# Optimization experiments

Hardware: AMD Instinct MI355X
Metric: run time of the kernel (lower is better)

## Reference

```python
import jax, jax.numpy as jnp
import numpy as np

B, L, D = 4, 2048, 1024
H, KD, VD = 16, 64, 64
EPS = 1e-5


def setup_inputs() -> dict:
    key = jax.random.key(0)
    ks = jax.random.split(key, 12)
    s_in = 1.0 / np.sqrt(D)
    s_out = 1.0 / np.sqrt(H * VD)
    return {
        "queries": jax.random.normal(ks[0], (B, L, D), dtype=jnp.float32),
        "Wq": jax.random.uniform(ks[1], (D, H * KD), jnp.float32, -s_in, s_in),
        "bq": jax.random.uniform(ks[2], (H * KD,), jnp.float32, -s_in, s_in),
        "Wk": jax.random.uniform(ks[3], (D, H * KD), jnp.float32, -s_in, s_in),
        "bk": jax.random.uniform(ks[4], (H * KD,), jnp.float32, -s_in, s_in),
        "Wv": jax.random.uniform(ks[5], (D, H * VD), jnp.float32, -s_in, s_in),
        "bv": jax.random.uniform(ks[6], (H * VD,), jnp.float32, -s_in, s_in),
        "Wo": jax.random.uniform(ks[7], (H * VD, D), jnp.float32, -s_out, s_out),
        "bo": jax.random.uniform(ks[8], (D,), jnp.float32, -s_out, s_out),
        "gamma": jnp.ones((D,), jnp.float32),
        "beta": jnp.zeros((D,), jnp.float32),
    }


def reference(queries, Wq, bq, Wk, bk, Wv, bv, Wo, bo, gamma, beta):
    # QKV projections -> [B, L, H, head_dim]
    q = (queries @ Wq + bq).reshape(B, L, H, KD)
    k = (queries @ Wk + bk).reshape(B, L, H, KD)
    v = (queries @ Wv + bv).reshape(B, L, H, VD)
    # scaled dot-product attention per head: scores [B, H, Lq, Lk]
    scores = jnp.einsum("bqhd,bkhd->bhqk", q, k) / np.sqrt(KD).astype(np.float32)
    attn = jax.nn.softmax(scores, axis=-1)
    out = jnp.einsum("bhqk,bkhd->bqhd", attn, v).reshape(B, L, H * VD)
    # out projection (dropout is identity in eval), residual + LayerNorm
    res = out @ Wo + bo + queries
    mu = jnp.mean(res, axis=-1, keepdims=True)
    var = jnp.var(res, axis=-1, keepdims=True)
    return (res - mu) / jnp.sqrt(var + EPS) * gamma + beta
```

## Files before the change

### kernel.cpp

```cpp
#include <hip/hip_runtime.h>
#include <hip/hip_bf16.h>

#define BATCH 4
#define SEQ   2048
#define DIM   1024
#define NHEAD 16
#define HDIM  64
#define EPS_LN 1e-5f
#define QSCALE 0.18033688011112042f

typedef __attribute__((ext_vector_type(8))) short short8;
typedef __attribute__((ext_vector_type(4))) float f32x4;

__device__ __forceinline__ unsigned short f2bf(float x) {
    __hip_bfloat16 h = __float2bfloat16(x);
    return *reinterpret_cast<unsigned short*>(&h);
}
__device__ __forceinline__ unsigned int pack2bf(float a, float b) {
    __hip_bfloat162 h = __float22bfloat162_rn(float2{a, b});
    return *reinterpret_cast<unsigned int*>(&h);
}

__device__ __forceinline__ void gl_lds16(const void* g, void* l) {
    __builtin_amdgcn_global_load_lds(
        (const __attribute__((address_space(1))) unsigned int*)g,
        (__attribute__((address_space(3))) unsigned int*)l,
        16, 0, 0);
}

__global__ __launch_bounds__(256) void convert_bf16(const float* __restrict__ in,
                                                    unsigned short* __restrict__ out)
{
    const int i = blockIdx.x * 256 + threadIdx.x;
    float4 v = ((const float4*)in)[i];
    ushort4 u;
    u.x = f2bf(v.x); u.y = f2bf(v.y); u.z = f2bf(v.z); u.w = f2bf(v.w);
    ((ushort4*)out)[i] = u;
}

__global__ __launch_bounds__(256) void transpose_convert4(const float* __restrict__ W0,
                                                          const float* __restrict__ W1,
                                                          const float* __restrict__ W2,
                                                          const float* __restrict__ W3,
                                                          unsigned short* __restrict__ Wqkvt,
                                                          unsigned short* __restrict__ Wot)
{
    __shared__ float Ts[64][65];
    const int z = blockIdx.z;
    const float* W = (z == 0) ? W0 : (z == 1) ? W1 : (z == 2) ? W2 : W3;
    unsigned short* Wt = (z == 3) ? Wot : (Wqkvt + (size_t)z * DIM * DIM);

    const int k0 = blockIdx.y * 64, n0 = blockIdx.x * 64;
    const int t = threadIdx.x;
    const int lr = t >> 2, lq = t & 3;

#pragma unroll
    for (int i = 0; i < 4; i++) {
        float4 v = *(const float4*)(W + (size_t)(k0 + lr) * DIM + n0 + (lq * 4 + i) * 4);
        Ts[lr][(lq * 4 + i) * 4 + 0] = v.x;
        Ts[lr][(lq * 4 + i) * 4 + 1] = v.y;
        Ts[lr][(lq * 4 + i) * 4 + 2] = v.z;
        Ts[lr][(lq * 4 + i) * 4 + 3] = v.w;
    }
    __syncthreads();
#pragma unroll
    for (int i = 0; i < 4; i++) {
        const int c = lq * 16 + i * 4;
        ushort4 u;
        u.x = f2bf(Ts[c + 0][lr]);
        u.y = f2bf(Ts[c + 1][lr]);
        u.z = f2bf(Ts[c + 2][lr]);
        u.w = f2bf(Ts[c + 3][lr]);
        *(ushort4*)(Wt + (size_t)(n0 + lr) * DIM + k0 + c) = u;
    }
}

__global__ __launch_bounds__(256) void gemm_qkv(const unsigned short* __restrict__ A,
                                                const unsigned short* __restrict__ Bt,
                                                const float* __restrict__ bq,
                                                const float* __restrict__ bk,
                                                const float* __restrict__ bv,
                                                unsigned short* __restrict__ Qbf,
                                                unsigned short* __restrict__ Kbf,
                                                unsigned short* __restrict__ Vtb)
{
    __shared__ __attribute__((aligned(16))) unsigned short As[128 * 32];
    __shared__ __attribute__((aligned(16))) unsigned short Bs[128 * 32];

    const int tid = threadIdx.x;
    const int w = tid >> 6, lane = tid & 63;
    const int col = lane & 15, quad = lane >> 4;
    const int wm = (w >> 1) * 64, wn = (w & 1) * 64;
    const int m0 = blockIdx.y * 128, n0 = blockIdx.x * 128;

    f32x4 acc[4][4] = {};
    const int srow = tid >> 2, sc4 = tid & 3;

    for (int k0 = 0; k0 < DIM; k0 += 32) {
        __syncthreads();
#pragma unroll
        for (int it = 0; it < 2; it++) {
            gl_lds16(A  + (size_t)(m0 + srow + it * 64) * DIM + k0 + sc4 * 8,
                     (char*)As + w * 1024 + it * 4096);
            gl_lds16(Bt + (size_t)(n0 + srow + it * 64) * DIM + k0 + sc4 * 8,
                     (char*)Bs + w * 1024 + it * 4096);
        }
        __syncthreads();

        short8 af[4], bf[4];
#pragma unroll
        for (int mt = 0; mt < 4; mt++) af[mt] = *(short8*)&As[(wm + mt * 16 + col) * 32 + quad * 8];
#pragma unroll
        for (int nt = 0; nt < 4; nt++) bf[nt] = *(short8*)&Bs[(wn + nt * 16 + col) * 32 + quad * 8];

#pragma unroll
        for (int mt = 0; mt < 4; mt++)
#pragma unroll
            for (int nt = 0; nt < 4; nt++)
                acc[mt][nt] = __builtin_amdgcn_mfma_f32_16x16x32_bf16(af[mt], bf[nt], acc[mt][nt], 0, 0, 0);
    }

    const int sector = n0 >> 10;
    const float* bias = (sector == 0) ? bq : (sector == 1) ? bk : bv;

#pragma unroll
    for (int nt = 0; nt < 4; nt++) {
        const int n = n0 + wn + nt * 16 + col;
        const int nloc = n - (sector << 10);
        const float bvv = bias[nloc];
#pragma unroll
        for (int mt = 0; mt < 4; mt++) {
            const int mbase = m0 + wm + mt * 16 + quad * 4;
            if (sector == 0) {
#pragma unroll
                for (int r = 0; r < 4; r++)
                    Qbf[(size_t)(mbase + r) * DIM + nloc] = f2bf((acc[mt][nt][r] + bvv) * QSCALE);
            } else if (sector == 1) {
#pragma unroll
                for (int r = 0; r < 4; r++)
                    Kbf[(size_t)(mbase + r) * DIM + nloc] = f2bf(acc[mt][nt][r] + bvv);
            } else {
                const int h = nloc >> 6, d = nloc & 63;
                const int b = mbase >> 11, l = mbase & 2047;
                ushort4 u;
                u.x = f2bf(acc[mt][nt][0] + bvv);
                u.y = f2bf(acc[mt][nt][1] + bvv);
                u.z = f2bf(acc[mt][nt][2] + bvv);
                u.w = f2bf(acc[mt][nt][3] + bvv);
                *(ushort4*)(Vtb + ((size_t)((b * NHEAD + h) * HDIM + d)) * SEQ + l) = u;
            }
        }
    }
}

__global__ __launch_bounds__(256) void gemm_out(const unsigned short* __restrict__ A,
                                                const unsigned short* __restrict__ Bt,
                                                const float* __restrict__ bias,
                                                const float* __restrict__ resid,
                                                float* __restrict__ Cout)
{
    __shared__ __attribute__((aligned(16))) unsigned short As[128 * 32];
    __shared__ __attribute__((aligned(16))) unsigned short Bs[128 * 32];

    const int tid = threadIdx.x;
    const int w = tid >> 6, lane = tid & 63;
    const int col = lane & 15, quad = lane >> 4;
    const int wm = (w >> 1) * 64, wn = (w & 1) * 64;
    const int m0 = blockIdx.y * 128, n0 = blockIdx.x * 128;

    f32x4 acc[4][4] = {};
    const int srow = tid >> 2, sc4 = tid & 3;

    for (int k0 = 0; k0 < DIM; k0 += 32) {
        __syncthreads();
#pragma unroll
        for (int it = 0; it < 2; it++) {
            gl_lds16(A  + (size_t)(m0 + srow + it * 64) * DIM + k0 + sc4 * 8,
                     (char*)As + w * 1024 + it * 4096);
            gl_lds16(Bt + (size_t)(n0 + srow + it * 64) * DIM + k0 + sc4 * 8,
                     (char*)Bs + w * 1024 + it * 4096);
        }
        __syncthreads();

        short8 af[4], bf[4];
#pragma unroll
        for (int mt = 0; mt < 4; mt++) af[mt] = *(short8*)&As[(wm + mt * 16 + col) * 32 + quad * 8];
#pragma unroll
        for (int nt = 0; nt < 4; nt++) bf[nt] = *(short8*)&Bs[(wn + nt * 16 + col) * 32 + quad * 8];

#pragma unroll
        for (int mt = 0; mt < 4; mt++)
#pragma unroll
            for (int nt = 0; nt < 4; nt++)
                acc[mt][nt] = __builtin_amdgcn_mfma_f32_16x16x32_bf16(af[mt], bf[nt], acc[mt][nt], 0, 0, 0);
    }

#pragma unroll
    for (int nt = 0; nt < 4; nt++) {
        const int n = n0 + wn + nt * 16 + col;
        const float bvv = bias[n];
#pragma unroll
        for (int mt = 0; mt < 4; mt++) {
            const int mbase = m0 + wm + mt * 16 + quad * 4;
#pragma unroll
            for (int r = 0; r < 4; r++) {
                const size_t off = (size_t)(mbase + r) * DIM + n;
                Cout[off] = acc[mt][nt][r] + bvv + resid[off];
            }
        }
    }
}

#define KP 72
__global__ __launch_bounds__(256) void attn_mfma(const unsigned short* __restrict__ Qb,
                                                 const unsigned short* __restrict__ Kb,
                                                 const unsigned short* __restrict__ Vt,
                                                 unsigned short* __restrict__ Ob)
{
    __shared__ __attribute__((aligned(16))) unsigned short Ks[64 * KP];
    __shared__ __attribute__((aligned(16))) unsigned short Vs[64 * KP];
    __shared__ __attribute__((aligned(16))) unsigned short Ps[4][32 * KP];

    const int tid = threadIdx.x;
    const int w = tid >> 6, lane = tid & 63;
    const int col = lane & 15, quad = lane >> 4;

    const int nqt = SEQ / 128;
    const int qt_ = blockIdx.x % nqt;
    const int h   = (blockIdx.x / nqt) % NHEAD;
    const int b   = blockIdx.x / (nqt * NHEAD);

    const int q0 = qt_ * 128 + w * 32;

    short8 qf[2][2];
#pragma unroll
    for (int qt = 0; qt < 2; qt++) {
        const size_t base = ((size_t)(b * SEQ) + q0 + qt * 16 + col) * DIM + h * HDIM + quad * 8;
        qf[qt][0] = *(const short8*)(Qb + base);
        qf[qt][1] = *(const short8*)(Qb + base + 32);
    }

    short8 onesf;
    {
        const short v = (col == 0) ? (short)0x3F80 : (short)0;
        onesf = short8{v, v, v, v, v, v, v, v};
    }

    f32x4 o[4][2] = {};
    f32x4 od[2]   = {};

    const size_t kbase0 = ((size_t)(b * SEQ)) * DIM + h * HDIM;
    const size_t vbase0 = ((size_t)((b * NHEAD + h) * HDIM)) * SEQ;

    const int srow = tid >> 3, sc = tid & 7;
    unsigned short* Pw = Ps[w];

    for (int kt = 0; kt < SEQ / 64; kt++) {
        __syncthreads();
#pragma unroll
        for (int it = 0; it < 2; it++) {
            const int row = srow + it * 32;
            *(int4*)&Ks[row * KP + sc * 8] = *(const int4*)(Kb + kbase0 + (size_t)(kt * 64 + row) * DIM + sc * 8);
            *(int4*)&Vs[row * KP + sc * 8] = *(const int4*)(Vt + vbase0 + (size_t)row * SEQ + kt * 64 + sc * 8);
        }
        __syncthreads();

#pragma unroll
        for (int nt = 0; nt < 4; nt++) {
            short8 kf0 = *(short8*)&Ks[(nt * 16 + col) * KP + quad * 8];
            short8 kf1 = *(short8*)&Ks[(nt * 16 + col) * KP + quad * 8 + 32];
#pragma unroll
            for (int qt = 0; qt < 2; qt++) {
                f32x4 s = {};
                s = __builtin_amdgcn_mfma_f32_16x16x32_bf16(kf0, qf[qt][0], s, 0, 0, 0);
                s = __builtin_amdgcn_mfma_f32_16x16x32_bf16(kf1, qf[qt][1], s, 0, 0, 0);
                const float p0 = __builtin_amdgcn_exp2f(s[0]);
                const float p1 = __builtin_amdgcn_exp2f(s[1]);
                const float p2 = __builtin_amdgcn_exp2f(s[2]);
                const float p3 = __builtin_amdgcn_exp2f(s[3]);
                uint2 pk;
                pk.x = pack2bf(p0, p1);
                pk.y = pack2bf(p2, p3);
                *(uint2*)&Pw[(qt * 16 + col) * KP + nt * 16 + quad * 4] = pk;
            }
        }

        short8 pf[2][2];
#pragma unroll
        for (int qt = 0; qt < 2; qt++) {
            pf[qt][0] = *(short8*)&Pw[(qt * 16 + col) * KP + quad * 8];
            pf[qt][1] = *(short8*)&Pw[(qt * 16 + col) * KP + quad * 8 + 32];
        }

#pragma unroll
        for (int qt = 0; qt < 2; qt++) {
            od[qt] = __builtin_amdgcn_mfma_f32_16x16x32_bf16(onesf, pf[qt][0], od[qt], 0, 0, 0);
            od[qt] = __builtin_amdgcn_mfma_f32_16x16x32_bf16(onesf, pf[qt][1], od[qt], 0, 0, 0);
        }

#pragma unroll
        for (int mt = 0; mt < 4; mt++) {
            short8 vf0 = *(short8*)&Vs[(mt * 16 + col) * KP + quad * 8];
            short8 vf1 = *(short8*)&Vs[(mt * 16 + col) * KP + quad * 8 + 32];
#pragma unroll
            for (int qt = 0; qt < 2; qt++) {
                o[mt][qt] = __builtin_amdgcn_mfma_f32_16x16x32_bf16(vf0, pf[qt][0], o[mt][qt], 0, 0, 0);
                o[mt][qt] = __builtin_amdgcn_mfma_f32_16x16x32_bf16(vf1, pf[qt][1], o[mt][qt], 0, 0, 0);
            }
        }
    }

#pragma unroll
    for (int qt = 0; qt < 2; qt++) {
        const float den = __shfl(od[qt][0], col);
        const float inv = 1.f / den;
        const size_t rowoff = ((size_t)(b * SEQ) + q0 + qt * 16 + col) * DIM + h * HDIM;
#pragma unroll
        for (int mt = 0; mt < 4; mt++) {
            ushort4 u;
            u.x = f2bf(o[mt][qt][0] * inv);
            u.y = f2bf(o[mt][qt][1] * inv);
            u.z = f2bf(o[mt][qt][2] * inv);
            u.w = f2bf(o[mt][qt][3] * inv);
            *(ushort4*)(Ob + rowoff + mt * 16 + quad * 4) = u;
        }
    }
}

__global__ __launch_bounds__(256) void layernorm_kernel(float* __restrict__ res,
                                                        const float* __restrict__ gamma,
                                                        const float* __restrict__ beta)
{
    const int tid = threadIdx.x;
    const int row = blockIdx.x;
    float4 xv = ((const float4*)(res + (size_t)row * DIM))[tid];

    float s  = xv.x + xv.y + xv.z + xv.w;
    float sq = xv.x * xv.x + xv.y * xv.y + xv.z * xv.z + xv.w * xv.w;
#pragma unroll
    for (int off = 32; off; off >>= 1) {
        s  += __shfl_xor(s, off);
        sq += __shfl_xor(sq, off);
    }
    __shared__ float sm[8];
    const int w = tid >> 6, lane = tid & 63;
    if (lane == 0) { sm[w] = s; sm[4 + w] = sq; }
    __syncthreads();
    const float st  = sm[0] + sm[1] + sm[2] + sm[3];
    const float sqt = sm[4] + sm[5] + sm[6] + sm[7];
    const float mu   = st * (1.f / DIM);
    const float var  = sqt * (1.f / DIM) - mu * mu;
    const float rstd = rsqrtf(var + EPS_LN);

    float4 g  = ((const float4*)gamma)[tid];
    float4 be = ((const float4*)beta)[tid];
    float4 o;
    o.x = (xv.x - mu) * rstd * g.x + be.x;
    o.y = (xv.y - mu) * rstd * g.y + be.y;
    o.z = (xv.z - mu) * rstd * g.z + be.z;
    o.w = (xv.w - mu) * rstd * g.w + be.w;
    ((float4*)(res + (size_t)row * DIM))[tid] = o;
}

extern "C" void kernel_launch(void* const* d_in, const int* in_sizes, int n_in,
                              void* d_out, int out_size, void* d_ws, size_t ws_size,
                              hipStream_t stream)
{
    const float* queries = (const float*)d_in[0];
    const float* Wq = (const float*)d_in[1];
    const float* bq = (const float*)d_in[2];
    const float* Wk = (const float*)d_in[3];
    const float* bk = (const float*)d_in[4];
    const float* Wv = (const float*)d_in[5];
    const float* bv = (const float*)d_in[6];
    const float* Wo = (const float*)d_in[7];
    const float* bo = (const float*)d_in[8];
    const float* gamma = (const float*)d_in[9];
    const float* beta  = (const float*)d_in[10];
    float* outp = (float*)d_out;

    const int M = BATCH * SEQ;
    const size_t BUF = (size_t)M * DIM;
    const size_t WSZ = (size_t)DIM * DIM;

    unsigned short* w0  = (unsigned short*)d_ws;
    unsigned short* qin = w0;
    unsigned short* Qbf = w0 + BUF;
    unsigned short* Kbf = w0 + 2 * BUF;
    unsigned short* Vtb = w0 + 3 * BUF;
    unsigned short* Wqkvt = w0 + 4 * BUF;
    unsigned short* Wot   = Wqkvt + 3 * WSZ;
    unsigned short* Obf = qin;

    dim3 blk(256);

    convert_bf16<<<BUF / 4 / 256, blk, 0, stream>>>(queries, qin);

    dim3 tgrid(DIM / 64, DIM / 64, 4);
    transpose_convert4<<<tgrid, blk, 0, stream>>>(Wq, Wk, Wv, Wo, Wqkvt, Wot);

    dim3 qkvgrid(3 * DIM / 128, M / 128);
    gemm_qkv<<<qkvgrid, blk, 0, stream>>>(qin, Wqkvt, bq, bk, bv, Qbf, Kbf, Vtb);

    attn_mfma<<<BATCH * NHEAD * (SEQ / 128), blk, 0, stream>>>(Qbf, Kbf, Vtb, Obf);

    dim3 ogrid(DIM / 128, M / 128);
    gemm_out<<<ogrid, blk, 0, stream>>>(Obf, Wot, bo, queries, outp);

    layernorm_kernel<<<M, blk, 0, stream>>>(outp, gamma, beta);
}
```

Before: 319.9 us.

## Merge prep kernels, prefetch K/V tiles into registers, reorder attention block mapping

Folds the bf16 conversion of queries into the weight transpose kernel as a fifth z-slice, saving one kernel launch. In attention, the next K/V tile is loaded into registers while the current tile is being computed, so global load latency overlaps MFMA work. The block index is remapped so that consecutive blocks cover different (batch, head) pairs for the same query tile. The prefetch adds register pressure, and the conversion slice uses a grid-stride loop over only 256 blocks.

```diff
diff --git a/kernel.cpp b/kernel.cpp
--- a/kernel.cpp
+++ b/kernel.cpp
@@ -28,30 +28,35 @@
         16, 0, 0);
 }
 
-__global__ __launch_bounds__(256) void convert_bf16(const float* __restrict__ in,
-                                                    unsigned short* __restrict__ out)
-{
-    const int i = blockIdx.x * 256 + threadIdx.x;
-    float4 v = ((const float4*)in)[i];
-    ushort4 u;
-    u.x = f2bf(v.x); u.y = f2bf(v.y); u.z = f2bf(v.z); u.w = f2bf(v.w);
-    ((ushort4*)out)[i] = u;
-}
-
-__global__ __launch_bounds__(256) void transpose_convert4(const float* __restrict__ W0,
-                                                          const float* __restrict__ W1,
-                                                          const float* __restrict__ W2,
-                                                          const float* __restrict__ W3,
-                                                          unsigned short* __restrict__ Wqkvt,
-                                                          unsigned short* __restrict__ Wot)
-{
+__global__ __launch_bounds__(256) void prep_kernel(const float* __restrict__ W0,
+                                                   const float* __restrict__ W1,
+                                                   const float* __restrict__ W2,
+                                                   const float* __restrict__ W3,
+                                                   const float* __restrict__ queries,
+                                                   unsigned short* __restrict__ Wqkvt,
+                                                   unsigned short* __restrict__ Wot,
+                                                   unsigned short* __restrict__ qout)
+{
+    const int z = blockIdx.z;
+    const int t = threadIdx.x;
+
+    if (z == 4) {
+        const int nthr = 16 * 16 * 256;
+        int i = (blockIdx.y * 16 + blockIdx.x) * 256 + t;
+        for (int it = 0; it < (BATCH * SEQ * DIM / 4) / nthr; it++, i += nthr) {
+            float4 v = ((const float4*)queries)[i];
+            ushort4 u;
+            u.x = f2bf(v.x); u.y = f2bf(v.y); u.z = f2bf(v.z); u.w = f2bf(v.w);
+            ((ushort4*)qout)[i] = u;
+        }
+        return;
+    }
+
     __shared__ float Ts[64][65];
-    const int z = blockIdx.z;
     const float* W = (z == 0) ? W0 : (z == 1) ? W1 : (z == 2) ? W2 : W3;
     unsigned short* Wt = (z == 3) ? Wot : (Wqkvt + (size_t)z * DIM * DIM);
 
     const int k0 = blockIdx.y * 64, n0 = blockIdx.x * 64;
-    const int t = threadIdx.x;
     const int lr = t >> 2, lq = t & 3;
 
 #pragma unroll
@@ -225,10 +230,10 @@
     const int w = tid >> 6, lane = tid & 63;
     const int col = lane & 15, quad = lane >> 4;
 
-    const int nqt = SEQ / 128;
-    const int qt_ = blockIdx.x % nqt;
-    const int h   = (blockIdx.x / nqt) % NHEAD;
-    const int b   = blockIdx.x / (nqt * NHEAD);
+    const int bh  = blockIdx.x & 63;
+    const int qt_ = blockIdx.x >> 6;
+    const int b   = bh >> 4;
+    const int h   = bh & 15;
 
     const int q0 = qt_ * 128 + w * 32;
 
@@ -255,15 +260,32 @@
     const int srow = tid >> 3, sc = tid & 7;
     unsigned short* Pw = Ps[w];
 
+    int4 kreg[2], vreg[2];
+#pragma unroll
+    for (int it = 0; it < 2; it++) {
+        const int row = srow + it * 32;
+        kreg[it] = *(const int4*)(Kb + kbase0 + (size_t)row * DIM + sc * 8);
+        vreg[it] = *(const int4*)(Vt + vbase0 + (size_t)row * SEQ + sc * 8);
+    }
+
     for (int kt = 0; kt < SEQ / 64; kt++) {
         __syncthreads();
 #pragma unroll
         for (int it = 0; it < 2; it++) {
             const int row = srow + it * 32;
-            *(int4*)&Ks[row * KP + sc * 8] = *(const int4*)(Kb + kbase0 + (size_t)(kt * 64 + row) * DIM + sc * 8);
-            *(int4*)&Vs[row * KP + sc * 8] = *(const int4*)(Vt + vbase0 + (size_t)row * SEQ + kt * 64 + sc * 8);
-        }
-        __syncthreads();
+            *(int4*)&Ks[row * KP + sc * 8] = kreg[it];
+            *(int4*)&Vs[row * KP + sc * 8] = vreg[it];
+        }
+        __syncthreads();
+
+        if (kt + 1 < SEQ / 64) {
+#pragma unroll
+            for (int it = 0; it < 2; it++) {
+                const int row = srow + it * 32;
+                kreg[it] = *(const int4*)(Kb + kbase0 + (size_t)((kt + 1) * 64 + row) * DIM + sc * 8);
+                vreg[it] = *(const int4*)(Vt + vbase0 + (size_t)row * SEQ + (kt + 1) * 64 + sc * 8);
+            }
+        }
 
 #pragma unroll
         for (int nt = 0; nt < 4; nt++) {
@@ -394,10 +416,8 @@
 
     dim3 blk(256);
 
-    convert_bf16<<<BUF / 4 / 256, blk, 0, stream>>>(queries, qin);
-
-    dim3 tgrid(DIM / 64, DIM / 64, 4);
-    transpose_convert4<<<tgrid, blk, 0, stream>>>(Wq, Wk, Wv, Wo, Wqkvt, Wot);
+    dim3 pgrid(DIM / 64, DIM / 64, 5);
+    prep_kernel<<<pgrid, blk, 0, stream>>>(Wq, Wk, Wv, Wo, queries, Wqkvt, Wot, qin);
 
     dim3 qkvgrid(3 * DIM / 128, M / 128);
     gemm_qkv<<<qkvgrid, blk, 0, stream>>>(qin, Wqkvt, bq, bk, bv, Qbf, Kbf, Vtb);
```

Result: slower. 428.5 us (+34.0%).
